# Kernel tuning notes

Measured on AMD Instinct MI355X. Metric: run time of the kernel, lower is better.

The kernel has to match this reference:

```python
import jax, jax.numpy as jnp
import numpy as np

N, E, D, C = 50000, 800000, 96, 40
L2_EPS = 1e-12  # tf.nn.l2_normalize epsilon


def setup_inputs() -> dict:
    key = jax.random.key(0)
    ks = jax.random.split(key, 8)
    row = jnp.sort(jax.random.randint(ks[0], (E,), 0, N, dtype=jnp.int32))
    col = jax.random.randint(ks[1], (E,), 0, N, dtype=jnp.int32)
    vals = jax.random.uniform(ks[2], (E,), dtype=jnp.float32)
    x = jax.random.normal(ks[3], (N, D), dtype=jnp.float32)
    w1 = jax.random.normal(ks[4], (D, D), dtype=jnp.float32) * 0.1
    w2 = jax.random.normal(ks[5], (D, D), dtype=jnp.float32) * 0.1
    wc = jax.random.normal(ks[6], (D, C), dtype=jnp.float32) * 0.1
    bc = jnp.zeros((C,), dtype=jnp.float32)
    return {"row": row, "col": col, "vals": vals, "x": x,
            "w1": w1, "w2": w2, "wc": wc, "bc": bc}


def _spmm(row, col, vals, h):
    # sparse A (coo: row, col, vals) @ dense h, via gather + segment_sum
    msg = vals[:, None] * h[col]            # [E, D]
    return jax.ops.segment_sum(msg, row, num_segments=N)


def reference(row, col, vals, x, w1, w2, wc, bc):
    h = x
    for w in (w1, w2):                       # GCNConv: act(A @ (h @ W)), no bias
        h = jax.nn.relu(_spmm(row, col, vals, h @ w))
    # tf.nn.l2_normalize(h, axis=1)
    sq = jnp.sum(h * h, axis=1, keepdims=True)
    out = h * jax.lax.rsqrt(jnp.maximum(sq, L2_EPS))
    probs = jax.nn.softmax(out @ wc + bc, axis=-1)
    return out, probs
```

## Files before the change

### kernel.cpp

```cpp
#include <hip/hip_runtime.h>
#include <hip/hip_bf16.h>

#define GN 50000
#define GE 800000
#define GD 96
#define GC 40
#define L2EPS 1e-12f
#define NBUCKET 6
#define BDIV 8334

typedef __attribute__((ext_vector_type(8))) short short8v;
typedef __attribute__((ext_vector_type(4))) float f32x4;

__device__ __forceinline__ unsigned f2bf(float x) {
    union { float f; unsigned u; } v; v.f = x;
    return (v.u + 0x7fffu + ((v.u >> 16) & 1u)) >> 16;
}
__device__ __forceinline__ float bflo(unsigned u) { return __uint_as_float(u << 16); }
__device__ __forceinline__ float bfhi(unsigned u) { return __uint_as_float(u & 0xffff0000u); }

__device__ __forceinline__ int lbound(const int* __restrict__ row, int key) {
    int lo = 0, hi = GE;
    while (lo < hi) {
        int mid = (lo + hi) >> 1;
        if (row[mid] < key) lo = mid + 1; else hi = mid;
    }
    return lo;
}

__global__ void prep_k(const int* __restrict__ row, const float* __restrict__ w1,
                       const float* __restrict__ w2, int* __restrict__ rp,
                       unsigned* __restrict__ Wb1, unsigned* __restrict__ Wb2) {
    int i = blockIdx.x * blockDim.x + threadIdx.x;
    if (i <= GN) rp[i] = lbound(row, i);
    if (i < 2 * 4608) {
        const float* W = (i < 4608) ? w1 : w2;
        unsigned* Wb   = (i < 4608) ? Wb1 : Wb2;
        int j = (i < 4608) ? i : i - 4608;
        int r = j & 3;
        int lane = (j >> 2) & 63;
        int frag = j >> 8;
        int nt = frag / 3, kt = frag - nt * 3;
        int c = nt * 16 + (lane & 15);
        int k = kt * 32 + (lane >> 4) * 8 + r * 2;
        Wb[j] = f2bf(W[k * GD + c]) | (f2bf(W[(k + 1) * GD + c]) << 16);
    }
}

__global__ void bucket_k(const int* __restrict__ rp, const int* __restrict__ col,
                         const float* __restrict__ vals, int2* __restrict__ ep) {
    int idx = blockIdx.x * blockDim.x + threadIdx.x;
    int n = idx >> 4;
    if (n >= GN) return;
    int l = idx & 15;
    int shift = (threadIdx.x & 63) & 48;
    unsigned lt_mask = (1u << l) - 1u;
    int e0 = rp[n], e1 = rp[n + 1];

    int cnt[NBUCKET] = {0, 0, 0, 0, 0, 0};
    for (int be = e0; be < e1; be += 16) {
        int e = be + l;
        bool valid = e < e1;
        int key = valid ? (col[e] / BDIV) : -1;
#pragma unroll
        for (int q = 0; q < NBUCKET; ++q) {
            unsigned m = (unsigned)(__ballot(key == q) >> shift) & 0xffffu;
            cnt[q] += __popc(m);
        }
    }
    int off[NBUCKET];
    off[0] = e0;
#pragma unroll
    for (int q = 1; q < NBUCKET; ++q) off[q] = off[q - 1] + cnt[q - 1];

    for (int be = e0; be < e1; be += 16) {
        int e = be + l;
        bool valid = e < e1;
        int c = valid ? col[e] : 0;
        float v = valid ? vals[e] : 0.f;
        int key = valid ? (c / BDIV) : -1;
#pragma unroll
        for (int q = 0; q < NBUCKET; ++q) {
            unsigned m = (unsigned)(__ballot(key == q) >> shift) & 0xffffu;
            if (key == q)
                ep[off[q] + __popc(m & lt_mask)] = make_int2(c, __float_as_int(v));
            off[q] += __popc(m);
        }
    }
}

__global__ __launch_bounds__(64) void gemm_mfma_k(const float* __restrict__ A,
                                                  const uint4* __restrict__ Wb,
                                                  unsigned short* __restrict__ O) {
    const int tile = blockIdx.x;
    const int l  = threadIdx.x;
    const int m  = l & 15;
    const int kg = l >> 4;

    const float* arow = A + (size_t)(tile * 16 + m) * GD + kg * 8;
    short8v ah[3], al[3];
#pragma unroll
    for (int kt = 0; kt < 3; ++kt) {
        const float4* ap = reinterpret_cast<const float4*>(arow + kt * 32);
        float4 x0 = ap[0], x1 = ap[1];
        uint4 H, L;
        H.x = f2bf(x0.x) | (f2bf(x0.y) << 16);
        H.y = f2bf(x0.z) | (f2bf(x0.w) << 16);
        H.z = f2bf(x1.x) | (f2bf(x1.y) << 16);
        H.w = f2bf(x1.z) | (f2bf(x1.w) << 16);
        L.x = f2bf(x0.x - bflo(H.x)) | (f2bf(x0.y - bfhi(H.x)) << 16);
        L.y = f2bf(x0.z - bflo(H.y)) | (f2bf(x0.w - bfhi(H.y)) << 16);
        L.z = f2bf(x1.x - bflo(H.z)) | (f2bf(x1.y - bfhi(H.z)) << 16);
        L.w = f2bf(x1.z - bflo(H.w)) | (f2bf(x1.w - bfhi(H.w)) << 16);
        union { uint4 u; short8v s; } ch, cl;
        ch.u = H; cl.u = L;
        ah[kt] = ch.s; al[kt] = cl.s;
    }

#pragma unroll
    for (int nt = 0; nt < 6; ++nt) {
        f32x4 acc = {0.f, 0.f, 0.f, 0.f};
#pragma unroll
        for (int kt = 0; kt < 3; ++kt) {
            union { uint4 u; short8v s; } b;
            b.u = Wb[(nt * 3 + kt) * 64 + l];
            acc = __builtin_amdgcn_mfma_f32_16x16x32_bf16(ah[kt], b.s, acc, 0, 0, 0);
            acc = __builtin_amdgcn_mfma_f32_16x16x32_bf16(al[kt], b.s, acc, 0, 0, 0);
        }
        int ccol = nt * 16 + m;
#pragma unroll
        for (int reg = 0; reg < 4; ++reg) {
            int rrow = tile * 16 + kg * 4 + reg;
            O[(size_t)rrow * GD + ccol] = (unsigned short)f2bf(acc[reg]);
        }
    }
}

#define FMA8(U, V)                                                    \
    a0 += (V) * bflo((U).x); a1 += (V) * bfhi((U).x);                 \
    a2 += (V) * bflo((U).y); a3 += (V) * bfhi((U).y);                 \
    a4 += (V) * bflo((U).z); a5 += (V) * bfhi((U).z);                 \
    a6 += (V) * bflo((U).w); a7 += (V) * bfhi((U).w);

__global__ void spmm_relu_k(const int* __restrict__ rp, const int2* __restrict__ ep,
                            const unsigned* __restrict__ Tb, float* __restrict__ H) {
    int idx = blockIdx.x * blockDim.x + threadIdx.x;
    int n = idx / 12;
    if (n >= GN) return;
    int t = idx - n * 12;
    int e0 = rp[n], e1 = rp[n + 1];
    float a0=0,a1=0,a2=0,a3=0,a4=0,a5=0,a6=0,a7=0;
    int e = e0;
    for (; e + 4 <= e1; e += 4) {
        int2 p0 = ep[e], p1 = ep[e+1], p2 = ep[e+2], p3 = ep[e+3];
        uint4 u0 = *reinterpret_cast<const uint4*>(Tb + (size_t)p0.x * 48 + t * 4);
        uint4 u1 = *reinterpret_cast<const uint4*>(Tb + (size_t)p1.x * 48 + t * 4);
        uint4 u2 = *reinterpret_cast<const uint4*>(Tb + (size_t)p2.x * 48 + t * 4);
        uint4 u3 = *reinterpret_cast<const uint4*>(Tb + (size_t)p3.x * 48 + t * 4);
        FMA8(u0, __int_as_float(p0.y)) FMA8(u1, __int_as_float(p1.y))
        FMA8(u2, __int_as_float(p2.y)) FMA8(u3, __int_as_float(p3.y))
    }
    for (; e < e1; ++e) {
        int2 p = ep[e];
        uint4 u = *reinterpret_cast<const uint4*>(Tb + (size_t)p.x * 48 + t * 4);
        FMA8(u, __int_as_float(p.y))
    }
    float4* hr = reinterpret_cast<float4*>(H + (size_t)n * GD + t * 8);
    hr[0] = make_float4(fmaxf(a0,0.f), fmaxf(a1,0.f), fmaxf(a2,0.f), fmaxf(a3,0.f));
    hr[1] = make_float4(fmaxf(a4,0.f), fmaxf(a5,0.f), fmaxf(a6,0.f), fmaxf(a7,0.f));
}

#define FMA12(U, W_, V)                                               \
    a0 += (V) * bflo((U).x); a1 += (V) * bfhi((U).x);                 \
    a2 += (V) * bflo((U).y); a3 += (V) * bfhi((U).y);                 \
    a4 += (V) * bflo((U).z); a5 += (V) * bfhi((U).z);                 \
    a6 += (V) * bflo((U).w); a7 += (V) * bfhi((U).w);                 \
    a8 += (V) * bflo((W_).x); a9 += (V) * bfhi((W_).x);               \
    a10 += (V) * bflo((W_).y); a11 += (V) * bfhi((W_).y);

__global__ void spmm_relu_norm_k(const int* __restrict__ rp, const int2* __restrict__ ep,
                                 const unsigned* __restrict__ Tb, float* __restrict__ H) {
    int idx = blockIdx.x * blockDim.x + threadIdx.x;
    int n = idx >> 3;
    if (n >= GN) return;
    int t = idx & 7;
    int e0 = rp[n], e1 = rp[n + 1];
    float a0=0,a1=0,a2=0,a3=0,a4=0,a5=0,a6=0,a7=0,a8=0,a9=0,a10=0,a11=0;
    int e = e0;
    for (; e + 2 <= e1; e += 2) {
        int2 p0 = ep[e], p1 = ep[e+1];
        const unsigned* r0p = Tb + (size_t)p0.x * 48;
        const unsigned* r1p = Tb + (size_t)p1.x * 48;
        uint4 u0 = *reinterpret_cast<const uint4*>(r0p + t * 4);
        uint2 w0 = *reinterpret_cast<const uint2*>(r0p + 32 + t * 2);
        uint4 u1 = *reinterpret_cast<const uint4*>(r1p + t * 4);
        uint2 w1 = *reinterpret_cast<const uint2*>(r1p + 32 + t * 2);
        FMA12(u0, w0, __int_as_float(p0.y)) FMA12(u1, w1, __int_as_float(p1.y))
    }
    for (; e < e1; ++e) {
        int2 p = ep[e];
        const unsigned* r = Tb + (size_t)p.x * 48;
        uint4 u = *reinterpret_cast<const uint4*>(r + t * 4);
        uint2 w = *reinterpret_cast<const uint2*>(r + 32 + t * 2);
        FMA12(u, w, __int_as_float(p.y))
    }
    a0=fmaxf(a0,0.f); a1=fmaxf(a1,0.f); a2=fmaxf(a2,0.f); a3=fmaxf(a3,0.f);
    a4=fmaxf(a4,0.f); a5=fmaxf(a5,0.f); a6=fmaxf(a6,0.f); a7=fmaxf(a7,0.f);
    a8=fmaxf(a8,0.f); a9=fmaxf(a9,0.f); a10=fmaxf(a10,0.f); a11=fmaxf(a11,0.f);
    float ss = a0*a0+a1*a1+a2*a2+a3*a3+a4*a4+a5*a5+a6*a6+a7*a7+a8*a8+a9*a9+a10*a10+a11*a11;
    ss += __shfl_xor(ss, 1);
    ss += __shfl_xor(ss, 2);
    ss += __shfl_xor(ss, 4);
    float s = rsqrtf(fmaxf(ss, L2EPS));
    a0*=s; a1*=s; a2*=s; a3*=s; a4*=s; a5*=s;
    a6*=s; a7*=s; a8*=s; a9*=s; a10*=s; a11*=s;
    float4* hr = reinterpret_cast<float4*>(H + (size_t)n * GD + t * 8);
    hr[0] = make_float4(a0, a1, a2, a3);
    hr[1] = make_float4(a4, a5, a6, a7);
    *reinterpret_cast<float4*>(H + (size_t)n * GD + 64 + t * 4) =
        make_float4(a8, a9, a10, a11);
}

__global__ void cls_gemm_k(const float* __restrict__ A, const float* __restrict__ WC,
                           const float* __restrict__ BC, float* __restrict__ L) {
    __shared__ float4 w4[GD * 10];
    const float4* W4 = reinterpret_cast<const float4*>(WC);
    for (int i = threadIdx.x; i < GD * 10; i += blockDim.x) w4[i] = W4[i];
    __syncthreads();
    int idx = blockIdx.x * blockDim.x + threadIdx.x;
    if (idx >= (GN / 4) * 10) return;
    int rq = idx / 10;
    int q  = idx - rq * 10;
    int r0 = rq * 4;
    const float* a = A + (size_t)r0 * GD;
    float4 acc0 = {0,0,0,0}, acc1 = {0,0,0,0}, acc2 = {0,0,0,0}, acc3 = {0,0,0,0};
    for (int k0 = 0; k0 < GD; k0 += 4) {
        float4 a0 = *reinterpret_cast<const float4*>(a + k0);
        float4 a1 = *reinterpret_cast<const float4*>(a + GD + k0);
        float4 a2 = *reinterpret_cast<const float4*>(a + 2 * GD + k0);
        float4 a3 = *reinterpret_cast<const float4*>(a + 3 * GD + k0);
#pragma unroll
        for (int kk = 0; kk < 4; ++kk) {
            float4 w = w4[(k0 + kk) * 10 + q];
            float s0 = ((const float*)&a0)[kk];
            float s1 = ((const float*)&a1)[kk];
            float s2 = ((const float*)&a2)[kk];
            float s3 = ((const float*)&a3)[kk];
            acc0.x += s0 * w.x; acc0.y += s0 * w.y; acc0.z += s0 * w.z; acc0.w += s0 * w.w;
            acc1.x += s1 * w.x; acc1.y += s1 * w.y; acc1.z += s1 * w.z; acc1.w += s1 * w.w;
            acc2.x += s2 * w.x; acc2.y += s2 * w.y; acc2.z += s2 * w.z; acc2.w += s2 * w.w;
            acc3.x += s3 * w.x; acc3.y += s3 * w.y; acc3.z += s3 * w.z; acc3.w += s3 * w.w;
        }
    }
    float4 b = *reinterpret_cast<const float4*>(BC + q * 4);
    acc0.x += b.x; acc0.y += b.y; acc0.z += b.z; acc0.w += b.w;
    acc1.x += b.x; acc1.y += b.y; acc1.z += b.z; acc1.w += b.w;
    acc2.x += b.x; acc2.y += b.y; acc2.z += b.z; acc2.w += b.w;
    acc3.x += b.x; acc3.y += b.y; acc3.z += b.z; acc3.w += b.w;
    float4* L4 = reinterpret_cast<float4*>(L);
    L4[(size_t)(r0 + 0) * 10 + q] = acc0;
    L4[(size_t)(r0 + 1) * 10 + q] = acc1;
    L4[(size_t)(r0 + 2) * 10 + q] = acc2;
    L4[(size_t)(r0 + 3) * 10 + q] = acc3;
}

__global__ void softmax_k(const float* __restrict__ L, float* __restrict__ PROBS) {
    int n = blockIdx.x * blockDim.x + threadIdx.x;
    if (n >= GN) return;
    const float4* lr = reinterpret_cast<const float4*>(L + (size_t)n * GC);
    float4 v[10];
#pragma unroll
    for (int i = 0; i < 10; ++i) v[i] = lr[i];
    float m = -1e30f;
#pragma unroll
    for (int i = 0; i < 10; ++i)
        m = fmaxf(m, fmaxf(fmaxf(v[i].x, v[i].y), fmaxf(v[i].z, v[i].w)));
    float sum = 0.f;
#pragma unroll
    for (int i = 0; i < 10; ++i) {
        v[i].x = __expf(v[i].x - m); v[i].y = __expf(v[i].y - m);
        v[i].z = __expf(v[i].z - m); v[i].w = __expf(v[i].w - m);
        sum += v[i].x + v[i].y + v[i].z + v[i].w;
    }
    float inv = 1.f / sum;
    float4* pr = reinterpret_cast<float4*>(PROBS + (size_t)n * GC);
#pragma unroll
    for (int i = 0; i < 10; ++i) {
        v[i].x *= inv; v[i].y *= inv; v[i].z *= inv; v[i].w *= inv;
        pr[i] = v[i];
    }
}

extern "C" void kernel_launch(void* const* d_in, const int* in_sizes, int n_in,
                              void* d_out, int out_size, void* d_ws, size_t ws_size,
                              hipStream_t stream) {
    const int*   row  = (const int*)d_in[0];
    const int*   col  = (const int*)d_in[1];
    const float* vals = (const float*)d_in[2];
    const float* x    = (const float*)d_in[3];
    const float* w1   = (const float*)d_in[4];
    const float* w2   = (const float*)d_in[5];
    const float* wc   = (const float*)d_in[6];
    const float* bc   = (const float*)d_in[7];

    float* out   = (float*)d_out;
    float* probs = out + (size_t)GN * GD;

    char*  ws  = (char*)d_ws;
    int*   rp  = (int*)ws;
    size_t off = (((size_t)(GN + 1) * 4) + 511) & ~(size_t)511;
    unsigned* buf = (unsigned*)(ws + off);
    off += (size_t)GN * GD * 4;
    off = (off + 511) & ~(size_t)511;
    int2* ep   = (int2*)(ws + off);
    off += (size_t)GE * 8;
    off = (off + 511) & ~(size_t)511;
    unsigned* Wb1 = (unsigned*)(ws + off);
    unsigned* Wb2 = Wb1 + 4608;

    prep_k<<<(GN + 1 + 255) / 256, 256, 0, stream>>>(row, w1, w2, rp, Wb1, Wb2);
    bucket_k<<<(GN * 16) / 256, 256, 0, stream>>>(rp, col, vals, ep);
    gemm_mfma_k<<<GN / 16, 64, 0, stream>>>(x, (const uint4*)Wb1, (unsigned short*)buf);
    spmm_relu_k<<<(GN * 12 + 255) / 256, 256, 0, stream>>>(rp, ep, buf, out);
    gemm_mfma_k<<<GN / 16, 64, 0, stream>>>(out, (const uint4*)Wb2, (unsigned short*)buf);
    spmm_relu_norm_k<<<(GN * 8 + 255) / 256, 256, 0, stream>>>(rp, ep, buf, out);
    cls_gemm_k<<<((GN / 4) * 10 + 255) / 256, 256, 0, stream>>>(out, wc, bc, (float*)buf);
    softmax_k<<<(GN + 255) / 256, 256, 0, stream>>>((float*)buf, probs);
}
```

Measured before the change: 109.5 us.

## Sort nodes by degree so SpMM wavefronts process rows of similar length

Builds a degree histogram during prep and a new place_k kernel that produces a permutation of nodes grouped by in-degree. Both SpMM kernels then map thread groups to nodes through this permutation, so lanes within a wavefront loop a similar number of times and divergence is reduced. In exchange it adds a memset, an extra kernel with atomics, and one more indirection. Output rows are written in scattered order, which loses write coalescing and locality across neighbouring nodes.

```diff
diff --git a/kernel.cpp b/kernel.cpp
--- a/kernel.cpp
+++ b/kernel.cpp
@@ -30,9 +30,18 @@
 
 __global__ void prep_k(const int* __restrict__ row, const float* __restrict__ w1,
                        const float* __restrict__ w2, int* __restrict__ rp,
-                       unsigned* __restrict__ Wb1, unsigned* __restrict__ Wb2) {
+                       int* __restrict__ hist, unsigned* __restrict__ Wb1,
+                       unsigned* __restrict__ Wb2) {
     int i = blockIdx.x * blockDim.x + threadIdx.x;
-    if (i <= GN) rp[i] = lbound(row, i);
+    if (i <= GN) {
+        int lo = lbound(row, i);
+        rp[i] = lo;
+        if (i < GN) {
+            int d = lbound(row, i + 1) - lo;
+            if (d > 127) d = 127;
+            atomicAdd(&hist[d], 1);
+        }
+    }
     if (i < 2 * 4608) {
         const float* W = (i < 4608) ? w1 : w2;
         unsigned* Wb   = (i < 4608) ? Wb1 : Wb2;
@@ -45,6 +54,17 @@
         int k = kt * 32 + (lane >> 4) * 8 + r * 2;
         Wb[j] = f2bf(W[k * GD + c]) | (f2bf(W[(k + 1) * GD + c]) << 16);
     }
+}
+
+__global__ void place_k(const int* __restrict__ rp, const int* __restrict__ hist,
+                        int* __restrict__ cnt, int* __restrict__ perm) {
+    int n = blockIdx.x * blockDim.x + threadIdx.x;
+    if (n >= GN) return;
+    int d = rp[n + 1] - rp[n];
+    if (d > 127) d = 127;
+    int base = 0;
+    for (int k = 0; k < d; ++k) base += hist[k];
+    perm[base + atomicAdd(&cnt[d], 1)] = n;
 }
 
 __global__ void bucket_k(const int* __restrict__ rp, const int* __restrict__ col,
@@ -142,12 +162,14 @@
     a4 += (V) * bflo((U).z); a5 += (V) * bfhi((U).z);                 \
     a6 += (V) * bflo((U).w); a7 += (V) * bfhi((U).w);
 
-__global__ void spmm_relu_k(const int* __restrict__ rp, const int2* __restrict__ ep,
+__global__ void spmm_relu_k(const int* __restrict__ rp, const int* __restrict__ perm,
+                            const int2* __restrict__ ep,
                             const unsigned* __restrict__ Tb, float* __restrict__ H) {
     int idx = blockIdx.x * blockDim.x + threadIdx.x;
-    int n = idx / 12;
-    if (n >= GN) return;
-    int t = idx - n * 12;
+    int gid = idx / 12;
+    if (gid >= GN) return;
+    int n = perm[gid];
+    int t = idx - gid * 12;
     int e0 = rp[n], e1 = rp[n + 1];
     float a0=0,a1=0,a2=0,a3=0,a4=0,a5=0,a6=0,a7=0;
     int e = e0;
@@ -178,11 +200,13 @@
     a8 += (V) * bflo((W_).x); a9 += (V) * bfhi((W_).x);               \
     a10 += (V) * bflo((W_).y); a11 += (V) * bfhi((W_).y);
 
-__global__ void spmm_relu_norm_k(const int* __restrict__ rp, const int2* __restrict__ ep,
+__global__ void spmm_relu_norm_k(const int* __restrict__ rp, const int* __restrict__ perm,
+                                 const int2* __restrict__ ep,
                                  const unsigned* __restrict__ Tb, float* __restrict__ H) {
     int idx = blockIdx.x * blockDim.x + threadIdx.x;
-    int n = idx >> 3;
-    if (n >= GN) return;
+    int gid = idx >> 3;
+    if (gid >= GN) return;
+    int n = perm[gid];
     int t = idx & 7;
     int e0 = rp[n], e1 = rp[n + 1];
     float a0=0,a1=0,a2=0,a3=0,a4=0,a5=0,a6=0,a7=0,a8=0,a9=0,a10=0,a11=0;
@@ -317,13 +341,22 @@
     off = (off + 511) & ~(size_t)511;
     unsigned* Wb1 = (unsigned*)(ws + off);
     unsigned* Wb2 = Wb1 + 4608;
-
-    prep_k<<<(GN + 1 + 255) / 256, 256, 0, stream>>>(row, w1, w2, rp, Wb1, Wb2);
+    off += 2 * 4608 * 4;
+    off = (off + 511) & ~(size_t)511;
+    int* hist = (int*)(ws + off);
+    int* cnt  = hist + 128;
+    off += 256 * 4;
+    off = (off + 511) & ~(size_t)511;
+    int* perm = (int*)(ws + off);
+
+    hipMemsetAsync(hist, 0, 256 * 4, stream);
+    prep_k<<<(GN + 1 + 255) / 256, 256, 0, stream>>>(row, w1, w2, rp, hist, Wb1, Wb2);
+    place_k<<<(GN + 255) / 256, 256, 0, stream>>>(rp, hist, cnt, perm);
     bucket_k<<<(GN * 16) / 256, 256, 0, stream>>>(rp, col, vals, ep);
     gemm_mfma_k<<<GN / 16, 64, 0, stream>>>(x, (const uint4*)Wb1, (unsigned short*)buf);
-    spmm_relu_k<<<(GN * 12 + 255) / 256, 256, 0, stream>>>(rp, ep, buf, out);
+    spmm_relu_k<<<(GN * 12 + 255) / 256, 256, 0, stream>>>(rp, perm, ep, buf, out);
     gemm_mfma_k<<<GN / 16, 64, 0, stream>>>(out, (const uint4*)Wb2, (unsigned short*)buf);
-    spmm_relu_norm_k<<<(GN * 8 + 255) / 256, 256, 0, stream>>>(rp, ep, buf, out);
+    spmm_relu_norm_k<<<(GN * 8 + 255) / 256, 256, 0, stream>>>(rp, perm, ep, buf, out);
     cls_gemm_k<<<((GN / 4) * 10 + 255) / 256, 256, 0, stream>>>(out, wc, bc, (float*)buf);
     softmax_k<<<(GN + 255) / 256, 256, 0, stream>>>((float*)buf, probs);
 }
```

Result: slower. 380.5 us (+247.6%).
